# Kernel tuning notes

Hardware: AMD Instinct MI355X
Metric: run time of the kernel (lower is better)

The kernel has to match this reference:

```python
import jax, jax.numpy as jnp
import numpy as np

E = 10        # ensemble_size
IN = 32       # input_dim
H = 256       # hidden_units
OUT = 24      # output_dim (head emits 2*OUT: mean and logvar)
B = 65536     # batch


def setup_inputs() -> dict:
    key = jax.random.key(0)
    ks = jax.random.split(key, 7)
    # Kaiming-uniform-ish init scale like torch Linear defaults
    def lin(k, fan_in, shape):
        bound = 1.0 / np.sqrt(fan_in)
        return jax.random.uniform(k, shape, jnp.float32, -bound, bound)
    return {
        "x":  jax.random.normal(ks[0], (B, IN), jnp.float32),
        "W1": lin(ks[1], IN, (E, IN, H)),
        "b1": lin(ks[2], IN, (E, H)),
        "W2": lin(ks[3], H, (E, H, H)),
        "b2": lin(ks[4], H, (E, H)),
        "W3": lin(ks[5], H, (E, H, 2 * OUT)),
        "b3": lin(ks[6], H, (E, 2 * OUT)),
    }


def reference(x, W1, b1, W2, b2, W3, b3):
    # Batched over ensemble axis e: one grouped GEMM per layer instead of
    # a Python loop of E small GEMMs.
    h = jax.nn.silu(jnp.einsum("bi,eih->ebh", x, W1) + b1[:, None, :])   # [E,B,H]
    h = jax.nn.silu(jnp.einsum("ebh,ehk->ebk", h, W2) + b2[:, None, :])  # [E,B,H]
    pred = jnp.einsum("ebh,eho->ebo", h, W3) + b3[:, None, :]            # [E,B,2*OUT]
    means = pred[..., :OUT]    # [E,B,OUT]
    logvars = pred[..., OUT:]  # [E,B,OUT]
    return (means, logvars)
```

## Files before the change

### kernel.cpp

```cpp
#include <hip/hip_runtime.h>

#define NEXP 10
#define IND 32
#define HD 256
#define OUTD 24
#define OUT2 48
#define BATCH 65536
#define NTHREADS 512
#define NWAVES 8
#define ROWS_PER_WAVE 32
#define ROWS_PER_BLOCK 256

typedef _Float16 half8 __attribute__((ext_vector_type(8)));
typedef float f32x16 __attribute__((ext_vector_type(16)));
typedef unsigned int u32;
typedef u32 u32x4 __attribute__((ext_vector_type(4)));

#define W1P_STRIDE 12288
#define W2P_STRIDE 69632
#define W3P_STRIDE 17408
#define W1P_OFF 0
#define W2P_OFF (NEXP * W1P_STRIDE)
#define W3P_OFF (W2P_OFF + NEXP * W2P_STRIDE)
#define PACK_PER_E (3*8*64 + 17*8*64 + 17*2*64)
#define PACK_TOTAL (NEXP * PACK_PER_E)

__device__ __forceinline__ void gl_lds16(const void* g, void* l) {
    __builtin_amdgcn_global_load_lds(
        (const __attribute__((address_space(1))) void*)g,
        (__attribute__((address_space(3))) void*)l, 16, 0, 0);
}

__device__ __forceinline__ int pi_map(int kb, int hi, int j) {
    return kb * 16 + hi * 4 + (j & 3) + 8 * (j >> 2);
}

__global__ void pack_weights(const float* __restrict__ W1, const float* __restrict__ b1,
                             const float* __restrict__ W2, const float* __restrict__ b2,
                             const float* __restrict__ W3, const float* __restrict__ b3,
                             _Float16* __restrict__ wp) {
    int gid = blockIdx.x * blockDim.x + threadIdx.x;
    if (gid >= PACK_TOTAL) return;
    int e = gid / PACK_PER_E;
    int r = gid % PACK_PER_E;
    half8 v;
    _Float16* dst;
    if (r < 1536) {
        int kc = r / 512, mt = (r / 64) % 8, lane = r % 64;
        int lo = lane & 31, hi = lane >> 5;
        int n1 = mt * 32 + lo;
#pragma unroll
        for (int j = 0; j < 8; ++j) {
            float x;
            if (kc < 2) { int k = kc * 16 + hi * 8 + j; x = W1[(e * IND + k) * HD + n1]; }
            else        { x = (hi == 0 && j == 0) ? b1[e * HD + n1] : 0.f; }
            v[j] = (_Float16)x;
        }
        dst = wp + W1P_OFF + (size_t)e * W1P_STRIDE + r * 8;
    } else if (r < 1536 + 8704) {
        int r2 = r - 1536;
        int kb = r2 / 512, mt = (r2 / 64) % 8, lane = r2 % 64;
        int lo = lane & 31, hi = lane >> 5;
        int n2 = mt * 32 + lo;
#pragma unroll
        for (int j = 0; j < 8; ++j) {
            float x;
            if (kb < 16) { int hid = pi_map(kb, hi, j); x = W2[(e * HD + hid) * HD + n2]; }
            else         { x = (hi == 0 && j == 0) ? b2[e * HD + n2] : 0.f; }
            v[j] = (_Float16)x;
        }
        dst = wp + W2P_OFF + (size_t)e * W2P_STRIDE + r2 * 8;
    } else {
        int r3 = r - 1536 - 8704;
        int kb = r3 / 128, mt = (r3 / 64) % 2, lane = r3 % 64;
        int lo = lane & 31, hi = lane >> 5;
        int n3 = mt * 32 + lo;
#pragma unroll
        for (int j = 0; j < 8; ++j) {
            float x = 0.f;
            if (n3 < OUT2) {
                if (kb < 16) { int hid = pi_map(kb, hi, j); x = W3[(e * HD + hid) * OUT2 + n3]; }
                else         { x = (hi == 0 && j == 0) ? b3[e * OUT2 + n3] : 0.f; }
            }
            v[j] = (_Float16)x;
        }
        dst = wp + W3P_OFF + (size_t)e * W3P_STRIDE + r3 * 8;
    }
    *(half8*)dst = v;
}

__device__ __forceinline__ float silu(float v) {
    return v * __builtin_amdgcn_rcpf(1.0f + __expf(-v));
}

__device__ __forceinline__ half8 pack_bfrag(const f32x16& a, int base) {
    float h0 = silu(a[base + 0]), h1 = silu(a[base + 1]);
    float h2 = silu(a[base + 2]), h3 = silu(a[base + 3]);
    float h4 = silu(a[base + 4]), h5 = silu(a[base + 5]);
    float h6 = silu(a[base + 6]), h7 = silu(a[base + 7]);
    u32x4 w;
    w[0] = __builtin_bit_cast(u32, __builtin_amdgcn_cvt_pkrtz(h0, h1));
    w[1] = __builtin_bit_cast(u32, __builtin_amdgcn_cvt_pkrtz(h2, h3));
    w[2] = __builtin_bit_cast(u32, __builtin_amdgcn_cvt_pkrtz(h4, h5));
    w[3] = __builtin_bit_cast(u32, __builtin_amdgcn_cvt_pkrtz(h6, h7));
    return __builtin_bit_cast(half8, w);
}

__global__ __launch_bounds__(NTHREADS, 2)
void fused_mlp(const float* __restrict__ x,
               const _Float16* __restrict__ wp,
               float* __restrict__ out) {
    __shared__ _Float16 w2s[128 * 512];

    const int tid = threadIdx.x;
    const int wave = tid >> 6, lane = tid & 63;
    const int lo = lane & 31, hi = lane >> 5;
    const int e = blockIdx.y;
    const int b0 = blockIdx.x * ROWS_PER_BLOCK + wave * ROWS_PER_WAVE;
    const int b = b0 + lo;

    const _Float16* w1pe = wp + W1P_OFF + (size_t)e * W1P_STRIDE;
    const _Float16* w2pe = wp + W2P_OFF + (size_t)e * W2P_STRIDE;
    const _Float16* w2bias = w2pe + 16 * 4096;
    const _Float16* w3pe = wp + W3P_OFF + (size_t)e * W3P_STRIDE;

#pragma unroll
    for (int i = 0; i < 16; ++i) {
        int fid = wave * 16 + i;
        gl_lds16(w2pe + fid * 512 + lane * 8, &w2s[fid * 512]);
    }

    const float* xr = x + (size_t)b * IND + hi * 8;
    float4 xa0 = *(const float4*)(xr);
    float4 xa1 = *(const float4*)(xr + 4);
    float4 xb0 = *(const float4*)(xr + 16);
    float4 xb1 = *(const float4*)(xr + 20);
    half8 xf[2];
    {
        u32x4 w;
        w[0] = __builtin_bit_cast(u32, __builtin_amdgcn_cvt_pkrtz(xa0.x, xa0.y));
        w[1] = __builtin_bit_cast(u32, __builtin_amdgcn_cvt_pkrtz(xa0.z, xa0.w));
        w[2] = __builtin_bit_cast(u32, __builtin_amdgcn_cvt_pkrtz(xa1.x, xa1.y));
        w[3] = __builtin_bit_cast(u32, __builtin_amdgcn_cvt_pkrtz(xa1.z, xa1.w));
        xf[0] = __builtin_bit_cast(half8, w);
        w[0] = __builtin_bit_cast(u32, __builtin_amdgcn_cvt_pkrtz(xb0.x, xb0.y));
        w[1] = __builtin_bit_cast(u32, __builtin_amdgcn_cvt_pkrtz(xb0.z, xb0.w));
        w[2] = __builtin_bit_cast(u32, __builtin_amdgcn_cvt_pkrtz(xb1.x, xb1.y));
        w[3] = __builtin_bit_cast(u32, __builtin_amdgcn_cvt_pkrtz(xb1.z, xb1.w));
        xf[1] = __builtin_bit_cast(half8, w);
    }
    half8 bb;
    {
        u32x4 w = {0u, 0u, 0u, 0u};
        w[0] = (hi == 0) ? 0x00003C00u : 0u;
        bb = __builtin_bit_cast(half8, w);
    }

    f32x16 acc1[8];
#pragma unroll
    for (int mt = 0; mt < 8; ++mt)
#pragma unroll
        for (int i = 0; i < 16; ++i) acc1[mt][i] = 0.f;

#pragma unroll
    for (int kc = 0; kc < 2; ++kc)
#pragma unroll
        for (int mt = 0; mt < 8; ++mt) {
            half8 a = *(const half8*)(w1pe + (kc * 8 + mt) * 512 + lane * 8);
            acc1[mt] = __builtin_amdgcn_mfma_f32_32x32x16_f16(a, xf[kc], acc1[mt], 0, 0, 0);
        }
#pragma unroll
    for (int mt = 0; mt < 8; ++mt) {
        half8 a = *(const half8*)(w1pe + (2 * 8 + mt) * 512 + lane * 8);
        acc1[mt] = __builtin_amdgcn_mfma_f32_32x32x16_f16(a, bb, acc1[mt], 0, 0, 0);
    }

    half8 bf[16];
#pragma unroll
    for (int kb = 0; kb < 16; ++kb)
        bf[kb] = pack_bfrag(acc1[kb >> 1], (kb & 1) * 8);

    __syncthreads();

    f32x16 acc2[8];
#pragma unroll
    for (int mt = 0; mt < 8; ++mt)
#pragma unroll
        for (int i = 0; i < 16; ++i) acc2[mt][i] = 0.f;

#pragma unroll
    for (int kb = 0; kb < 16; ++kb)
#pragma unroll
        for (int mt = 0; mt < 8; ++mt) {
            half8 a = *(const half8*)&w2s[(kb * 8 + mt) * 512 + lane * 8];
            acc2[mt] = __builtin_amdgcn_mfma_f32_32x32x16_f16(a, bf[kb], acc2[mt], 0, 0, 0);
        }
#pragma unroll
    for (int mt = 0; mt < 8; ++mt) {
        half8 a = *(const half8*)(w2bias + mt * 512 + lane * 8);
        acc2[mt] = __builtin_amdgcn_mfma_f32_32x32x16_f16(a, bb, acc2[mt], 0, 0, 0);
    }

    half8 bf2[16];
#pragma unroll
    for (int kb = 0; kb < 16; ++kb)
        bf2[kb] = pack_bfrag(acc2[kb >> 1], (kb & 1) * 8);

    f32x16 acc3[2];
#pragma unroll
    for (int mt = 0; mt < 2; ++mt)
#pragma unroll
        for (int i = 0; i < 16; ++i) acc3[mt][i] = 0.f;

#pragma unroll
    for (int kb = 0; kb < 16; ++kb)
#pragma unroll
        for (int mt = 0; mt < 2; ++mt) {
            half8 a = *(const half8*)(w3pe + (kb * 2 + mt) * 512 + lane * 8);
            acc3[mt] = __builtin_amdgcn_mfma_f32_32x32x16_f16(a, bf2[kb], acc3[mt], 0, 0, 0);
        }
#pragma unroll
    for (int mt = 0; mt < 2; ++mt) {
        half8 a = *(const half8*)(w3pe + (16 * 2 + mt) * 512 + lane * 8);
        acc3[mt] = __builtin_amdgcn_mfma_f32_32x32x16_f16(a, bb, acc3[mt], 0, 0, 0);
    }

    const size_t lv_base = (size_t)NEXP * BATCH * OUTD;
#pragma unroll
    for (int mt = 0; mt < 2; ++mt)
#pragma unroll
        for (int q = 0; q < 4; ++q) {
            int n = mt * 32 + q * 8 + 4 * hi;
            if (n >= OUT2) continue;
            float4 v = {acc3[mt][q * 4 + 0], acc3[mt][q * 4 + 1],
                        acc3[mt][q * 4 + 2], acc3[mt][q * 4 + 3]};
            size_t off = (n < OUTD)
                ? (((size_t)e * BATCH + b) * OUTD + n)
                : (lv_base + ((size_t)e * BATCH + b) * OUTD + (n - OUTD));
            *(float4*)&out[off] = v;
        }
}

extern "C" void kernel_launch(void* const* d_in, const int* in_sizes, int n_in,
                              void* d_out, int out_size, void* d_ws, size_t ws_size,
                              hipStream_t stream) {
    (void)in_sizes; (void)n_in; (void)out_size; (void)ws_size;
    const float* x  = (const float*)d_in[0];
    const float* W1 = (const float*)d_in[1];
    const float* b1 = (const float*)d_in[2];
    const float* W2 = (const float*)d_in[3];
    const float* b2 = (const float*)d_in[4];
    const float* W3 = (const float*)d_in[5];
    const float* b3 = (const float*)d_in[6];
    float* out = (float*)d_out;
    _Float16* wp = (_Float16*)d_ws;

    pack_weights<<<(PACK_TOTAL + 255) / 256, 256, 0, stream>>>(W1, b1, W2, b2, W3, b3, wp);
    dim3 grid(BATCH / ROWS_PER_BLOCK, NEXP);
    fused_mlp<<<grid, NTHREADS, 0, stream>>>(x, wp, out);
}
```

Baseline: 378.6 us.

## Double-buffer W2 in LDS chunks with smaller blocks and MFMA priority

```diff
diff --git a/kernel.cpp b/kernel.cpp
--- a/kernel.cpp
+++ b/kernel.cpp
@@ -6,10 +6,10 @@
 #define OUTD 24
 #define OUT2 48
 #define BATCH 65536
-#define NTHREADS 512
-#define NWAVES 8
+#define NTHREADS 256
+#define NWAVES 4
 #define ROWS_PER_WAVE 32
-#define ROWS_PER_BLOCK 256
+#define ROWS_PER_BLOCK 128
 
 typedef _Float16 half8 __attribute__((ext_vector_type(8)));
 typedef float f32x16 __attribute__((ext_vector_type(16)));
@@ -106,29 +106,33 @@
     return __builtin_bit_cast(half8, w);
 }
 
+__device__ __forceinline__ void stage_chunk(const _Float16* __restrict__ w2pe,
+                                            _Float16* dstbuf, int c, int tid) {
+    const _Float16* src = w2pe + c * 16384;
+#pragma unroll
+    for (int i = 0; i < 8; ++i)
+        gl_lds16(src + (i * 256 + tid) * 8, dstbuf + (i * 256 + tid) * 8);
+}
+
 __global__ __launch_bounds__(NTHREADS, 2)
 void fused_mlp(const float* __restrict__ x,
                const _Float16* __restrict__ wp,
                float* __restrict__ out) {
-    __shared__ _Float16 w2s[128 * 512];
+    __shared__ _Float16 w2s[2][16384];
 
     const int tid = threadIdx.x;
     const int wave = tid >> 6, lane = tid & 63;
     const int lo = lane & 31, hi = lane >> 5;
     const int e = blockIdx.y;
-    const int b0 = blockIdx.x * ROWS_PER_BLOCK + wave * ROWS_PER_WAVE;
-    const int b = b0 + lo;
+    const int b = blockIdx.x * ROWS_PER_BLOCK + wave * ROWS_PER_WAVE + lo;
 
     const _Float16* w1pe = wp + W1P_OFF + (size_t)e * W1P_STRIDE;
     const _Float16* w2pe = wp + W2P_OFF + (size_t)e * W2P_STRIDE;
     const _Float16* w2bias = w2pe + 16 * 4096;
     const _Float16* w3pe = wp + W3P_OFF + (size_t)e * W3P_STRIDE;
 
-#pragma unroll
-    for (int i = 0; i < 16; ++i) {
-        int fid = wave * 16 + i;
-        gl_lds16(w2pe + fid * 512 + lane * 8, &w2s[fid * 512]);
-    }
+    stage_chunk(w2pe, w2s[0], 0, tid);
+    stage_chunk(w2pe, w2s[1], 1, tid);
 
     const float* xr = x + (size_t)b * IND + hi * 8;
     float4 xa0 = *(const float4*)(xr);
@@ -162,6 +166,7 @@
 #pragma unroll
         for (int i = 0; i < 16; ++i) acc1[mt][i] = 0.f;
 
+    __builtin_amdgcn_s_setprio(1);
 #pragma unroll
     for (int kc = 0; kc < 2; ++kc)
 #pragma unroll
@@ -174,27 +179,38 @@
         half8 a = *(const half8*)(w1pe + (2 * 8 + mt) * 512 + lane * 8);
         acc1[mt] = __builtin_amdgcn_mfma_f32_32x32x16_f16(a, bb, acc1[mt], 0, 0, 0);
     }
+    __builtin_amdgcn_s_setprio(0);
 
     half8 bf[16];
 #pragma unroll
     for (int kb = 0; kb < 16; ++kb)
         bf[kb] = pack_bfrag(acc1[kb >> 1], (kb & 1) * 8);
 
+    f32x16 acc2[8];
+#pragma unroll
+    for (int mt = 0; mt < 8; ++mt)
+#pragma unroll
+        for (int i = 0; i < 16; ++i) acc2[mt][i] = 0.f;
+
     __syncthreads();
 
-    f32x16 acc2[8];
-#pragma unroll
-    for (int mt = 0; mt < 8; ++mt)
-#pragma unroll
-        for (int i = 0; i < 16; ++i) acc2[mt][i] = 0.f;
-
-#pragma unroll
-    for (int kb = 0; kb < 16; ++kb)
-#pragma unroll
-        for (int mt = 0; mt < 8; ++mt) {
-            half8 a = *(const half8*)&w2s[(kb * 8 + mt) * 512 + lane * 8];
-            acc2[mt] = __builtin_amdgcn_mfma_f32_32x32x16_f16(a, bf[kb], acc2[mt], 0, 0, 0);
-        }
+#pragma unroll
+    for (int c = 0; c < 4; ++c) {
+        const _Float16* buf = w2s[c & 1];
+        __builtin_amdgcn_s_setprio(1);
+#pragma unroll
+        for (int kbl = 0; kbl < 4; ++kbl)
+#pragma unroll
+            for (int mt = 0; mt < 8; ++mt) {
+                half8 a = *(const half8*)(buf + (kbl * 8 + mt) * 512 + lane * 8);
+                acc2[mt] = __builtin_amdgcn_mfma_f32_32x32x16_f16(a, bf[c * 4 + kbl], acc2[mt], 0, 0, 0);
+            }
+        __builtin_amdgcn_s_setprio(0);
+        if (c < 3) {
+            __syncthreads();
+            if (c < 2) stage_chunk(w2pe, w2s[c & 1], c + 2, tid);
+        }
+    }
 #pragma unroll
     for (int mt = 0; mt < 8; ++mt) {
         half8 a = *(const half8*)(w2bias + mt * 512 + lane * 8);
@@ -212,6 +228,7 @@
 #pragma unroll
         for (int i = 0; i < 16; ++i) acc3[mt][i] = 0.f;
 
+    __builtin_amdgcn_s_setprio(1);
 #pragma unroll
     for (int kb = 0; kb < 16; ++kb)
 #pragma unroll
@@ -224,6 +241,7 @@
         half8 a = *(const half8*)(w3pe + (16 * 2 + mt) * 512 + lane * 8);
         acc3[mt] = __builtin_amdgcn_mfma_f32_32x32x16_f16(a, bb, acc3[mt], 0, 0, 0);
     }
+    __builtin_amdgcn_s_setprio(0);
 
     const size_t lv_base = (size_t)NEXP * BATCH * OUTD;
 #pragma unroll
```

After: 315.4 us. 1.2x faster.
